# Optimization experiments

Hardware: AMD Instinct MI355X
Metric: run time of the kernel (lower is better)

## Reference

```python
import jax, jax.numpy as jnp
import numpy as np

B, L, D, E, K, DFF = 2, 2048, 1024, 8, 2, 4096


def setup_inputs() -> dict:
    key = jax.random.key(0)
    kx, kr, kg, ku, kd = jax.random.split(key, 5)
    scale = 0.02
    return {
        "x": jax.random.normal(kx, (B, L, D), dtype=jnp.float32),
        "Wr": jax.random.normal(kr, (E, D), dtype=jnp.float32) * scale,   # router: logits = x @ Wr.T
        "Wg": jax.random.normal(kg, (E, DFF, D), dtype=jnp.float32) * scale,  # gate proj per expert
        "Wu": jax.random.normal(ku, (E, DFF, D), dtype=jnp.float32) * scale,  # up proj per expert
        "Wd": jax.random.normal(kd, (E, D, DFF), dtype=jnp.float32) * scale,  # down proj per expert
    }


def reference(x, Wr, Wg, Wu, Wd):
    Bb, Ll, Dd = x.shape
    T = Bb * Ll
    xt = x.reshape(T, Dd)                                   # [T, D]
    logits = jnp.einsum("td,ed->te", xt, Wr)                # router logits [T, E]
    scores = jax.nn.softmax(logits, axis=-1)
    k_scores, k_ids = jax.lax.top_k(scores, K)              # [T, K]
    eps = jnp.finfo(x.dtype).eps
    k_w = k_scores / (k_scores.sum(axis=-1, keepdims=True) + eps)  # renormalized top-k weights
    # combine[t, e] = sum_k k_w[t, k] * (k_ids[t, k] == e)
    combine = jnp.sum(jax.nn.one_hot(k_ids, E, dtype=x.dtype) * k_w[..., None], axis=1)  # [T, E]
    # GluMLP per expert, computed densely over all tokens (reference form)
    g = jnp.einsum("td,efd->etf", xt, Wg)                   # [E, T, DFF]
    u = jnp.einsum("td,efd->etf", xt, Wu)                   # [E, T, DFF]
    h = jax.nn.relu(g) * u
    out_e = jnp.einsum("etf,edf->etd", h, Wd)               # [E, T, D]
    out = jnp.einsum("te,etd->td", combine, out_e)          # weighted combine [T, D]
    return out.reshape(Bb, Ll, Dd)
```

## Files before the change

### kernel.cpp

```cpp
#include <hip/hip_runtime.h>
#include <hip/hip_bf16.h>

#define Tt 4096
#define Dd 1024
#define Ee 8
#define Kk 2
#define Ff 4096

using f32x4  = __attribute__((ext_vector_type(4))) float;
using bf16x8 = __attribute__((ext_vector_type(8))) short;

__device__ __forceinline__ unsigned short f2bf(float f) {
    union { float fp; unsigned int u; } v; v.fp = f;
    unsigned int u = v.u;
    return (unsigned short)((u + 0x7FFFu + ((u >> 16) & 1u)) >> 16);
}

__device__ __forceinline__ float b2f(unsigned short u) {
    union { float f; unsigned int i; } v; v.i = (unsigned)u << 16; return v.f;
}

__device__ __forceinline__ void gl16(const void* g, void* l) {
    __builtin_amdgcn_global_load_lds(
        (const __attribute__((address_space(1))) void*)g,
        (__attribute__((address_space(3))) void*)l, 16, 0, 0);
}

__global__ void router_kernel(const float* __restrict__ x, const float* __restrict__ Wr,
                              int* __restrict__ ids, float* __restrict__ wts,
                              int* __restrict__ counts, unsigned short* __restrict__ xb) {
    const int t = blockIdx.x;
    const int lane = threadIdx.x;
    const float* xr = x + (size_t)t * Dd + lane * 16;
    float xv[16];
#pragma unroll
    for (int i = 0; i < 4; ++i) *(float4*)(xv + 4 * i) = *(const float4*)(xr + 4 * i);
    uint4 o0, o1;
    o0.x = (unsigned)f2bf(xv[0])  | ((unsigned)f2bf(xv[1])  << 16);
    o0.y = (unsigned)f2bf(xv[2])  | ((unsigned)f2bf(xv[3])  << 16);
    o0.z = (unsigned)f2bf(xv[4])  | ((unsigned)f2bf(xv[5])  << 16);
    o0.w = (unsigned)f2bf(xv[6])  | ((unsigned)f2bf(xv[7])  << 16);
    o1.x = (unsigned)f2bf(xv[8])  | ((unsigned)f2bf(xv[9])  << 16);
    o1.y = (unsigned)f2bf(xv[10]) | ((unsigned)f2bf(xv[11]) << 16);
    o1.z = (unsigned)f2bf(xv[12]) | ((unsigned)f2bf(xv[13]) << 16);
    o1.w = (unsigned)f2bf(xv[14]) | ((unsigned)f2bf(xv[15]) << 16);
    unsigned short* xo = xb + (size_t)t * Dd + lane * 16;
    *(uint4*)(xo) = o0;
    *(uint4*)(xo + 8) = o1;

    double dot[Ee];
#pragma unroll
    for (int e = 0; e < Ee; ++e) {
        const float* wr = Wr + e * Dd + lane * 16;
        double s = 0.0;
#pragma unroll
        for (int i = 0; i < 16; ++i) s += (double)xv[i] * (double)wr[i];
        dot[e] = s;
    }
#pragma unroll
    for (int off = 32; off >= 1; off >>= 1) {
#pragma unroll
        for (int e = 0; e < Ee; ++e) dot[e] += __shfl_xor(dot[e], off, 64);
    }
    if (lane == 0) {
        float lg[Ee];
#pragma unroll
        for (int e = 0; e < Ee; ++e) lg[e] = (float)dot[e];
        float m = lg[0];
        for (int e = 1; e < Ee; ++e) m = fmaxf(m, lg[e]);
        float ex[Ee]; float sum = 0.f;
        for (int e = 0; e < Ee; ++e) { ex[e] = expf(lg[e] - m); sum += ex[e]; }
        float s0 = -1.f, s1 = -1.f; int i0 = 0, i1 = 0;
        for (int e = 0; e < Ee; ++e) {
            float s = ex[e];
            if (s > s0)      { s1 = s0; i1 = i0; s0 = s; i0 = e; }
            else if (s > s1) { s1 = s; i1 = e; }
        }
        float inv = 1.f / sum;
        float sc0 = s0 * inv, sc1 = s1 * inv;
        float den = sc0 + sc1 + 1.1920929e-7f;
        ids[2 * t] = i0; ids[2 * t + 1] = i1;
        wts[2 * t] = sc0 / den; wts[2 * t + 1] = sc1 / den;
        atomicAdd(&counts[i0], 1);
        atomicAdd(&counts[i1], 1);
    }
}

__global__ void cvt_wgu(const float* __restrict__ Wg, const float* __restrict__ Wu,
                        unsigned short* __restrict__ Wgu) {
    size_t tid = (size_t)blockIdx.x * blockDim.x + threadIdx.x;
    size_t row = tid >> 7;
    int dc  = (int)(tid & 127);
    int e   = (int)(row >> 13);
    int j   = (int)(row & 8191);
    int fg = j >> 5, s = (j >> 4) & 1, fi = j & 15;
    int f  = fg * 16 + fi;
    const float* src = (s ? Wu : Wg) + ((size_t)e * Ff + f) * Dd + dc * 8;
    float4 a = *(const float4*)(src);
    float4 b = *(const float4*)(src + 4);
    uint4 o;
    o.x = (unsigned)f2bf(a.x) | ((unsigned)f2bf(a.y) << 16);
    o.y = (unsigned)f2bf(a.z) | ((unsigned)f2bf(a.w) << 16);
    o.z = (unsigned)f2bf(b.x) | ((unsigned)f2bf(b.y) << 16);
    o.w = (unsigned)f2bf(b.z) | ((unsigned)f2bf(b.w) << 16);
    *(uint4*)(Wgu + row * Dd + dc * 8) = o;
}

__global__ void scan_kernel(const int* __restrict__ counts, int* __restrict__ cursor,
                            int* __restrict__ eoff) {
    if (threadIdx.x == 0) {
        int acc = 0;
        for (int e = 0; e < Ee; ++e) { eoff[e] = acc; cursor[e] = acc; acc += counts[e]; }
        eoff[Ee] = acc;
    }
}

__global__ void scatter_kernel(const int* __restrict__ ids,
                               int* __restrict__ cursor, int* __restrict__ rows) {
    int t = blockIdx.x * blockDim.x + threadIdx.x;
    if (t >= Tt) return;
#pragma unroll
    for (int k = 0; k < Kk; ++k) {
        int e = ids[2 * t + k];
        int pos = atomicAdd(&cursor[e], 1);
        rows[pos] = 2 * t + k;
    }
}


#define MFMA_BF16(a, b, c) __builtin_amdgcn_mfma_f32_16x16x32_bf16(a, b, c, 0, 0, 0)

template<bool G2>
__device__ __forceinline__ void gemm_body(unsigned short* Ls,
                                          const unsigned short* __restrict__ Abase,
                                          const unsigned short* __restrict__ Bbase,
                                          const int* __restrict__ eoff,
                                          const int* __restrict__ rows,
                                          unsigned short* __restrict__ H,
                                          unsigned short* __restrict__ partial) {
    constexpr int KLEN = G2 ? Ff : Dd;
    constexpr int NT   = 16;
    const int e   = blockIdx.z;
    const int off = eoff[e];
    const int ne  = eoff[e + 1] - off;
    const int by  = blockIdx.y;
    const int my  = G2 ? (by >> 2) : by;
    const int sK  = G2 ? (by & 3) : 0;
    const int koff = sK * 1024;
    const int m0  = my * 256;
    if (m0 >= ne) return;
    const int n0  = blockIdx.x * 256;

    const int tid  = threadIdx.x;
    const int lane = tid & 63;
    const int w    = tid >> 6;
    const int wr   = w >> 2;
    const int wc   = w & 3;
    const int lr   = lane & 15;
    const int lc   = lane >> 4;

    const int sr = lane >> 3;
    const int cA = (lane & 7) ^ sr;
    int asrc[4];
#pragma unroll
    for (int qq = 0; qq < 4; ++qq) {
        int rr = m0 + qq * 64 + w * 8 + sr;
        if (rr > ne - 1) rr = ne - 1;
        asrc[qq] = (G2 ? (off + rr) : (rows[off + rr] >> 1)) * KLEN + cA * 8;
    }
    const unsigned short* Bp = Bbase + (size_t)e * (G2 ? (size_t)Dd * Ff : (size_t)8192 * Dd);
    int bsrc[4];
#pragma unroll
    for (int qq = 0; qq < 4; ++qq) {
        int rN = n0 + qq * 64 + w * 8 + sr;
        bsrc[qq] = rN * KLEN + cA * 8;
    }

    auto STAGE_A = [&](int T, int Hh) {
        const int bo_ = (T & 1) * 32768; const int kt_ = koff + T * 64;
        gl16(Abase + asrc[2 * Hh]     + kt_, Ls + bo_ + (2 * Hh)     * 4096 + w * 512);
        gl16(Abase + asrc[2 * Hh + 1] + kt_, Ls + bo_ + (2 * Hh + 1) * 4096 + w * 512);
    };
    auto STAGE_B = [&](int T, int Hh) {
        const int bo_ = (T & 1) * 32768 + 16384; const int kt_ = koff + T * 64;
        gl16(Bp + bsrc[2 * Hh]     + kt_, Ls + bo_ + (2 * Hh)     * 4096 + w * 512);
        gl16(Bp + bsrc[2 * Hh + 1] + kt_, Ls + bo_ + (2 * Hh + 1) * 4096 + w * 512);
    };

    const int ccx0 = ((0 * 4 + lc) ^ (lr & 7)) * 8;
    const int ccx1 = ((1 * 4 + lc) ^ (lr & 7)) * 8;
    const int aB = wr * 8192 + lr * 64;
    const int bB = 16384 + wc * 4096 + lr * 64;

    f32x4 acc[8][4];
#pragma unroll
    for (int m = 0; m < 8; ++m)
#pragma unroll
        for (int n = 0; n < 4; ++n) acc[m][n] = (f32x4){0.f, 0.f, 0.f, 0.f};

    STAGE_A(0, 0); STAGE_A(0, 1); STAGE_B(0, 0); STAGE_B(0, 1);
    STAGE_A(1, 0); STAGE_A(1, 1);
    asm volatile("s_waitcnt vmcnt(4)" ::: "memory");
    __builtin_amdgcn_sched_barrier(0);
    __builtin_amdgcn_s_barrier();

    bf16x8 a0[8], a1[8], b0[4], b1[4];

    for (int t = 0; t < NT; ++t) {
        const int bo = (t & 1) * 32768;
#pragma unroll
        for (int m = 0; m < 8; ++m) a0[m] = *(const bf16x8*)(Ls + bo + aB + m * 1024 + ccx0);
#pragma unroll
        for (int n = 0; n < 4; ++n) b0[n] = *(const bf16x8*)(Ls + bo + bB + n * 1024 + ccx0);
        if (t + 1 < NT) STAGE_B(t + 1, 0);
        __builtin_amdgcn_s_barrier();
        asm volatile("s_waitcnt lgkmcnt(0)" ::: "memory");
        __builtin_amdgcn_sched_barrier(0);
        __builtin_amdgcn_s_setprio(1);
#pragma unroll
        for (int m = 0; m < 8; ++m) {
            acc[m][0] = MFMA_BF16(a0[m], b0[0], acc[m][0]);
            acc[m][1] = MFMA_BF16(a0[m], b0[1], acc[m][1]);
        }
        __builtin_amdgcn_s_setprio(0);
        __builtin_amdgcn_s_barrier();
#pragma unroll
        for (int m = 0; m < 8; ++m) a1[m] = *(const bf16x8*)(Ls + bo + aB + m * 1024 + ccx1);
        if (t + 1 < NT) STAGE_B(t + 1, 1);
        __builtin_amdgcn_s_barrier();
        __builtin_amdgcn_s_setprio(1);
#pragma unroll
        for (int m = 0; m < 8; ++m) {
            acc[m][2] = MFMA_BF16(a0[m], b0[2], acc[m][2]);
            acc[m][3] = MFMA_BF16(a0[m], b0[3], acc[m][3]);
        }
        __builtin_amdgcn_s_setprio(0);
        asm volatile("s_waitcnt lgkmcnt(0)" ::: "memory");
        __builtin_amdgcn_sched_barrier(0);
        __builtin_amdgcn_s_barrier();
#pragma unroll
        for (int n = 0; n < 4; ++n) b1[n] = *(const bf16x8*)(Ls + bo + bB + n * 1024 + ccx1);
        if (t + 2 < NT) STAGE_A(t + 2, 0);
        __builtin_amdgcn_s_barrier();
        asm volatile("s_waitcnt lgkmcnt(0)" ::: "memory");
        __builtin_amdgcn_sched_barrier(0);
        __builtin_amdgcn_s_setprio(1);
#pragma unroll
        for (int m = 0; m < 8; ++m) {
            acc[m][0] = MFMA_BF16(a1[m], b1[0], acc[m][0]);
            acc[m][1] = MFMA_BF16(a1[m], b1[1], acc[m][1]);
        }
        __builtin_amdgcn_s_setprio(0);
        __builtin_amdgcn_s_barrier();
        if (t + 2 < NT) STAGE_A(t + 2, 1);
        __builtin_amdgcn_s_setprio(1);
#pragma unroll
        for (int m = 0; m < 8; ++m) {
            acc[m][2] = MFMA_BF16(a1[m], b1[2], acc[m][2]);
            acc[m][3] = MFMA_BF16(a1[m], b1[3], acc[m][3]);
        }
        __builtin_amdgcn_s_setprio(0);
        if (t + 2 < NT) { asm volatile("s_waitcnt vmcnt(4)" ::: "memory"); }
        else            { asm volatile("s_waitcnt vmcnt(0)" ::: "memory"); }
        __builtin_amdgcn_sched_barrier(0);
        __builtin_amdgcn_s_barrier();
    }

    if constexpr (!G2) {
        const int fg16 = ((n0 + wc * 64) >> 5) * 16 + lr;
#pragma unroll
        for (int m = 0; m < 8; ++m) {
            const int itok = m0 + wr * 128 + m * 16 + lc * 4;
#pragma unroll
            for (int r = 0; r < 4; ++r) {
                const int i = itok + r;
                if (i < ne) {
                    unsigned short* hp = H + (size_t)(off + i) * Ff;
#pragma unroll
                    for (int np = 0; np < 2; ++np) {
                        const float g = acc[m][2 * np][r];
                        const float u = acc[m][2 * np + 1][r];
                        hp[fg16 + np * 16] = f2bf(fmaxf(g, 0.f) * u);
                    }
                }
            }
        }
    } else {
        const int dbase = n0 + wc * 64;
#pragma unroll
        for (int m = 0; m < 8; ++m) {
            const int ib = m0 + wr * 128 + m * 16 + lc * 4;
#pragma unroll
            for (int r = 0; r < 4; ++r) {
                const int i = ib + r;
                if (i < ne) {
                    const int tr = rows[off + i];
                    unsigned short* op = partial + ((size_t)sK * 8192 + tr) * Dd + dbase + lr;
#pragma unroll
                    for (int n = 0; n < 4; ++n) op[n * 16] = f2bf(acc[m][n][r]);
                }
            }
        }
    }
}

__global__ __launch_bounds__(512, 1)
void g1_moe(const unsigned short* __restrict__ xb, const unsigned short* __restrict__ Wgu,
            const int* __restrict__ eoff, const int* __restrict__ rows,
            unsigned short* __restrict__ H,
            const float* __restrict__ Wd, unsigned short* __restrict__ Wdb) {
    __shared__ __align__(16) unsigned short Ls[65536];
    gemm_body<false>(Ls, xb, Wgu, eoff, rows, H, nullptr);
    const int fb = blockIdx.x + gridDim.x * (blockIdx.y + gridDim.y * blockIdx.z);
    const size_t base = (size_t)fb * 8192;
#pragma unroll
    for (int it = 0; it < 2; ++it) {
        const size_t i = base + (size_t)it * 4096 + threadIdx.x * 8;
        float4 a = *(const float4*)(Wd + i);
        float4 b = *(const float4*)(Wd + i + 4);
        uint4 o;
        o.x = (unsigned)f2bf(a.x) | ((unsigned)f2bf(a.y) << 16);
        o.y = (unsigned)f2bf(a.z) | ((unsigned)f2bf(a.w) << 16);
        o.z = (unsigned)f2bf(b.x) | ((unsigned)f2bf(b.y) << 16);
        o.w = (unsigned)f2bf(b.z) | ((unsigned)f2bf(b.w) << 16);
        *(uint4*)(Wdb + i) = o;
    }
}

__global__ __launch_bounds__(512, 1)
void g2_moe(const unsigned short* __restrict__ H, const unsigned short* __restrict__ Wdb,
            const int* __restrict__ eoff, const int* __restrict__ rows,
            unsigned short* __restrict__ partial) {
    __shared__ __align__(16) unsigned short Ls[65536];
    gemm_body<true>(Ls, H, Wdb, eoff, rows, nullptr, partial);
}

__global__ void reduce_kernel(const unsigned short* __restrict__ P, const float* __restrict__ wts,
                              float* __restrict__ out) {
    const size_t idx = (size_t)blockIdx.x * blockDim.x + threadIdx.x;
    const size_t t  = idx >> 7;
    const int   dq  = (int)(idx & 127);
    const float w0 = wts[2 * t], w1 = wts[2 * t + 1];
    float sa[8] = {0.f}, sb[8] = {0.f};
#pragma unroll
    for (int s = 0; s < 4; ++s) {
        bf16x8 a = *(const bf16x8*)(P + ((size_t)s * 8192 + 2 * t)     * Dd + dq * 8);
        bf16x8 b = *(const bf16x8*)(P + ((size_t)s * 8192 + 2 * t + 1) * Dd + dq * 8);
#pragma unroll
        for (int j = 0; j < 8; ++j) {
            sa[j] += b2f((unsigned short)a[j]);
            sb[j] += b2f((unsigned short)b[j]);
        }
    }
    float o[8];
#pragma unroll
    for (int j = 0; j < 8; ++j) o[j] = w0 * sa[j] + w1 * sb[j];
    float* op = out + t * Dd + dq * 8;
    *(float4*)(op)     = (float4){o[0], o[1], o[2], o[3]};
    *(float4*)(op + 4) = (float4){o[4], o[5], o[6], o[7]};
}

extern "C" void kernel_launch(void* const* d_in, const int* in_sizes, int n_in,
                              void* d_out, int out_size, void* d_ws, size_t ws_size,
                              hipStream_t stream) {
    const float* x  = (const float*)d_in[0];
    const float* Wr = (const float*)d_in[1];
    const float* Wg = (const float*)d_in[2];
    const float* Wu = (const float*)d_in[3];
    const float* Wd = (const float*)d_in[4];
    float* out = (float*)d_out;
    char* ws = (char*)d_ws;

    const size_t WELEM    = (size_t)Ee * Ff * Dd;
    const size_t OFF_IDS  = 256;
    const size_t OFF_WTS  = OFF_IDS  + (size_t)Tt * 2 * 4;
    const size_t OFF_ROWS = OFF_WTS  + (size_t)Tt * 2 * 4;
    const size_t OFF_ROWW = OFF_ROWS + (size_t)Tt * Kk * 4;
    const size_t OFF_XB   = OFF_ROWW + (size_t)Tt * Kk * 4;
    const size_t OFF_H    = OFF_XB   + (size_t)Tt * Dd * 2;
    const size_t OFF_WGU  = OFF_H    + (size_t)Tt * Kk * Ff * 2;
    const size_t OFF_WD   = OFF_WGU  + WELEM * 2 * 2;
    const size_t NEED     = OFF_WD   + WELEM * 2;
    if (ws_size < NEED) return;

    int* counts = (int*)ws;
    int* cursor = (int*)(ws + 32);
    int* eoff   = (int*)(ws + 64);
    int* ids    = (int*)(ws + OFF_IDS);
    float* wts  = (float*)(ws + OFF_WTS);
    int* rows   = (int*)(ws + OFF_ROWS);
    unsigned short* xb  = (unsigned short*)(ws + OFF_XB);
    unsigned short* H   = (unsigned short*)(ws + OFF_H);
    unsigned short* Wgu = (unsigned short*)(ws + OFF_WGU);
    unsigned short* Wdb = (unsigned short*)(ws + OFF_WD);
    unsigned short* partial = (unsigned short*)(ws + OFF_WGU);

    hipMemsetAsync(ws, 0, 256, stream);

    router_kernel  <<<Tt, 64, 0, stream>>>(x, Wr, ids, wts, counts, xb);
    scan_kernel    <<<1, 64, 0, stream>>>(counts, cursor, eoff);
    scatter_kernel <<<Tt / 256, 256, 0, stream>>>(ids, cursor, rows);

    cvt_wgu        <<<32768, 256, 0, stream>>>(Wg, Wu, Wgu);

    g1_moe <<<dim3(2 * Ff / 256, Tt / 256, Ee), 512, 0, stream>>>(
        xb, Wgu, eoff, rows, H, Wd, Wdb);
    g2_moe <<<dim3(Dd / 256, 20, Ee), 512, 0, stream>>>(
        H, Wdb, eoff, rows, partial);

    reduce_kernel  <<<(Tt * Dd / 8) / 256, 256, 0, stream>>>(partial, wts, out);
}
```

Measured before the change: 486.5 us.

## Merge scan and scatter kernels and make MoE GEMM blocks loop over row tiles

```diff
diff --git a/kernel.cpp b/kernel.cpp
--- a/kernel.cpp
+++ b/kernel.cpp
@@ -106,24 +106,22 @@
     *(uint4*)(Wgu + row * Dd + dc * 8) = o;
 }
 
-__global__ void scan_kernel(const int* __restrict__ counts, int* __restrict__ cursor,
-                            int* __restrict__ eoff) {
+__global__ void scan_scatter_kernel(const int* __restrict__ counts, const int* __restrict__ ids,
+                                    int* __restrict__ cursor, int* __restrict__ eoff,
+                                    int* __restrict__ rows) {
     if (threadIdx.x == 0) {
         int acc = 0;
         for (int e = 0; e < Ee; ++e) { eoff[e] = acc; cursor[e] = acc; acc += counts[e]; }
         eoff[Ee] = acc;
     }
-}
-
-__global__ void scatter_kernel(const int* __restrict__ ids,
-                               int* __restrict__ cursor, int* __restrict__ rows) {
-    int t = blockIdx.x * blockDim.x + threadIdx.x;
-    if (t >= Tt) return;
-#pragma unroll
-    for (int k = 0; k < Kk; ++k) {
-        int e = ids[2 * t + k];
-        int pos = atomicAdd(&cursor[e], 1);
-        rows[pos] = 2 * t + k;
+    __syncthreads();
+    for (int t = threadIdx.x; t < Tt; t += blockDim.x) {
+#pragma unroll
+        for (int k = 0; k < Kk; ++k) {
+            int e = ids[2 * t + k];
+            int pos = atomicAdd(&cursor[e], 1);
+            rows[pos] = 2 * t + k;
+        }
     }
 }
 
@@ -134,21 +132,13 @@
 __device__ __forceinline__ void gemm_body(unsigned short* Ls,
                                           const unsigned short* __restrict__ Abase,
                                           const unsigned short* __restrict__ Bbase,
-                                          const int* __restrict__ eoff,
                                           const int* __restrict__ rows,
                                           unsigned short* __restrict__ H,
-                                          unsigned short* __restrict__ partial) {
+                                          unsigned short* __restrict__ partial,
+                                          int e, int off, int ne, int m0, int sK) {
     constexpr int KLEN = G2 ? Ff : Dd;
     constexpr int NT   = 16;
-    const int e   = blockIdx.z;
-    const int off = eoff[e];
-    const int ne  = eoff[e + 1] - off;
-    const int by  = blockIdx.y;
-    const int my  = G2 ? (by >> 2) : by;
-    const int sK  = G2 ? (by & 3) : 0;
-    const int koff = sK * 1024;
-    const int m0  = my * 256;
-    if (m0 >= ne) return;
+    const int koff = sK << 10;
     const int n0  = blockIdx.x * 256;
 
     const int tid  = threadIdx.x;
@@ -302,6 +292,7 @@
             }
         }
     }
+    __builtin_amdgcn_s_barrier();
 }
 
 __global__ __launch_bounds__(512, 1)
@@ -310,11 +301,15 @@
             unsigned short* __restrict__ H,
             const float* __restrict__ Wd, unsigned short* __restrict__ Wdb) {
     __shared__ __align__(16) unsigned short Ls[65536];
-    gemm_body<false>(Ls, xb, Wgu, eoff, rows, H, nullptr);
+    const int e   = blockIdx.z;
+    const int off = eoff[e];
+    const int ne  = eoff[e + 1] - off;
+    for (int my = blockIdx.y; my * 256 < ne; my += 8)
+        gemm_body<false>(Ls, xb, Wgu, rows, H, nullptr, e, off, ne, my * 256, 0);
     const int fb = blockIdx.x + gridDim.x * (blockIdx.y + gridDim.y * blockIdx.z);
-    const size_t base = (size_t)fb * 8192;
-#pragma unroll
-    for (int it = 0; it < 2; ++it) {
+    const size_t base = (size_t)fb * 16384;
+#pragma unroll
+    for (int it = 0; it < 4; ++it) {
         const size_t i = base + (size_t)it * 4096 + threadIdx.x * 8;
         float4 a = *(const float4*)(Wd + i);
         float4 b = *(const float4*)(Wd + i + 4);
@@ -332,7 +327,12 @@
             const int* __restrict__ eoff, const int* __restrict__ rows,
             unsigned short* __restrict__ partial) {
     __shared__ __align__(16) unsigned short Ls[65536];
-    gemm_body<true>(Ls, H, Wdb, eoff, rows, nullptr, partial);
+    const int e   = blockIdx.z;
+    const int off = eoff[e];
+    const int ne  = eoff[e + 1] - off;
+    const int sK  = blockIdx.y & 3;
+    for (int my = blockIdx.y >> 2; my * 256 < ne; my += 5)
+        gemm_body<true>(Ls, H, Wdb, rows, nullptr, partial, e, off, ne, my * 256, sK);
 }
 
 __global__ void reduce_kernel(const unsigned short* __restrict__ P, const float* __restrict__ wts,
@@ -397,16 +397,15 @@
 
     hipMemsetAsync(ws, 0, 256, stream);
 
-    router_kernel  <<<Tt, 64, 0, stream>>>(x, Wr, ids, wts, counts, xb);
-    scan_kernel    <<<1, 64, 0, stream>>>(counts, cursor, eoff);
-    scatter_kernel <<<Tt / 256, 256, 0, stream>>>(ids, cursor, rows);
-
-    cvt_wgu        <<<32768, 256, 0, stream>>>(Wg, Wu, Wgu);
-
-    g1_moe <<<dim3(2 * Ff / 256, Tt / 256, Ee), 512, 0, stream>>>(
+    router_kernel      <<<Tt, 64, 0, stream>>>(x, Wr, ids, wts, counts, xb);
+    scan_scatter_kernel<<<1, 256, 0, stream>>>(counts, ids, cursor, eoff, rows);
+
+    cvt_wgu            <<<32768, 256, 0, stream>>>(Wg, Wu, Wgu);
+
+    g1_moe <<<dim3(2 * Ff / 256, 8, Ee), 512, 0, stream>>>(
         xb, Wgu, eoff, rows, H, Wd, Wdb);
     g2_moe <<<dim3(Dd / 256, 20, Ee), 512, 0, stream>>>(
         H, Wdb, eoff, rows, partial);
 
-    reduce_kernel  <<<(Tt * Dd / 8) / 256, 256, 0, stream>>>(partial, wts, out);
-}
+    reduce_kernel <<<(Tt * Dd / 8) / 256, 256, 0, stream>>>(partial, wts, out);
+}
```

After: 510.2 us. +4.9%, slower.
